# Performance work log

Hardware: AMD Instinct MI355X
Metric: run time of the kernel (lower is better)

The kernel has to match this reference:

```python
import jax, jax.numpy as jnp
import numpy as np

B, L, D, H = 2, 2048, 1024, 16
HD = D // H


def setup_inputs() -> dict:
    key = jax.random.key(0)
    ks = jax.random.split(key, 13)
    s = 0.02
    return {
        "x": jax.random.normal(ks[0], (B, L, D), jnp.float32),
        "pos_emb": jax.random.normal(ks[1], (1, L, D), jnp.float32),
        "Wq": jax.random.normal(ks[2], (D, D), jnp.float32) * s,
        "bq": jax.random.normal(ks[3], (D,), jnp.float32) * s,
        "Wk": jax.random.normal(ks[4], (D, D), jnp.float32) * s,
        "bk": jax.random.normal(ks[5], (D,), jnp.float32) * s,
        "Wv": jax.random.normal(ks[6], (D, D), jnp.float32) * s,
        "bv": jax.random.normal(ks[7], (D,), jnp.float32) * s,
        "Wpos": jax.random.normal(ks[8], (D, D), jnp.float32) * s,
        "pos_bias_u": jax.random.normal(ks[9], (H, HD), jnp.float32) * s,
        "pos_bias_v": jax.random.normal(ks[10], (H, HD), jnp.float32) * s,
        "Wo": jax.random.normal(ks[11], (D, D), jnp.float32) * s,
        "bo": jax.random.normal(ks[12], (D,), jnp.float32) * s,
    }


def _rel_shift(x):
    # x: (b, h, L, L) -> Transformer-XL relative shift
    b, h, q, k = x.shape
    x = jnp.pad(x, ((0, 0), (0, 0), (0, 0), (1, 0)))  # (b,h,L,L+1)
    x = x.reshape(b, h, k + 1, q)                      # (b,h,L+1,L)
    return x[:, :, 1:, :]                              # (b,h,L,L)


def reference(x, pos_emb, Wq, bq, Wk, bk, Wv, bv, Wpos, pos_bias_u, pos_bias_v, Wo, bo):
    b, seq, d = x.shape
    h, hd = pos_bias_u.shape
    scale = hd ** (-0.5)

    def proj(inp, W, bias=None):
        y = inp @ W.T
        if bias is not None:
            y = y + bias
        return y.reshape(inp.shape[0], seq, h, hd).transpose(0, 2, 1, 3)

    q = proj(x, Wq, bq)            # (b,h,L,hd)
    k = proj(x, Wk, bk)
    v = proj(x, Wv, bv)
    p = proj(pos_emb, Wpos)        # (1,h,L,hd)

    q_u = q + pos_bias_u[None, :, None, :]
    ac = jnp.einsum("bhqd,bhkd->bhqk", q_u, k)
    q_v = q + pos_bias_v[None, :, None, :]
    bd = jnp.matmul(q_v, jnp.swapaxes(p, -1, -2))  # broadcasts over batch
    bd = _rel_shift(bd)

    attn = jax.nn.softmax((ac + bd) * scale, axis=-1)
    out = jnp.einsum("bhqk,bhkd->bhqd", attn, v)
    out = out.transpose(0, 2, 1, 3).reshape(b, seq, d)
    return out @ Wo.T + bo
```

## Files before the change

### kernel.cpp

```cpp
#include <hip/hip_runtime.h>
#include <hip/hip_bf16.h>

constexpr int Lq = 2048;
constexpr int Dm = 1024;
constexpr int Hh = 16;
constexpr int HD = 64;

typedef __bf16 v8bf __attribute__((ext_vector_type(8)));
typedef short  v4s  __attribute__((ext_vector_type(4)));
typedef float  v4f  __attribute__((ext_vector_type(4)));

#define DEV static __device__ __forceinline__

DEV short f2bf(float f) {
  return (short)__builtin_bit_cast(unsigned short, __float2bfloat16(f));
}

DEV v4f MFMA(v8bf a, v8bf b, v4f c) {
  return __builtin_amdgcn_mfma_f32_16x16x32_bf16(a, b, c, 0, 0, 0);
}

template<int CTRL>
DEV float dppf(float x) {
  return __builtin_bit_cast(float, __builtin_amdgcn_update_dpp(
      0, __builtin_bit_cast(int, x), CTRL, 0xF, 0xF, true));
}
DEV float rowmax16(float x) {
  x = fmaxf(x, dppf<0xB1>(x));
  x = fmaxf(x, dppf<0x4E>(x));
  x = fmaxf(x, dppf<0x141>(x));
  x = fmaxf(x, dppf<0x140>(x));
  return x;
}

DEV float bperm(int byteaddr, float x) {
  return __builtin_bit_cast(float,
      __builtin_amdgcn_ds_bpermute(byteaddr, __builtin_bit_cast(int, x)));
}

#if __has_builtin(__builtin_amdgcn_exp2f)
DEV float exp2g(float x) { return __builtin_amdgcn_exp2f(x); }
#else
DEV float exp2g(float x) { return exp2f(x); }
#endif

DEV v4s cvt4(float4 v) {
  v4s w; w[0] = f2bf(v.x); w[1] = f2bf(v.y); w[2] = f2bf(v.z); w[3] = f2bf(v.w);
  return w;
}

__launch_bounds__(256)
__global__ void cvt_bf16(const float* __restrict__ in, short* __restrict__ out,
                         int n8)
{
  int i = blockIdx.x * 256 + threadIdx.x;
  if (i >= n8) return;
  float4 a = *(const float4*)(in + (size_t)i * 8);
  float4 b = *(const float4*)(in + (size_t)i * 8 + 4);
  *(v4s*)(out + (size_t)i * 8)     = cvt4(a);
  *(v4s*)(out + (size_t)i * 8 + 4) = cvt4(b);
}

__launch_bounds__(256)
__global__ void gemm_qkvp(const short* __restrict__ xb,
                          const short* __restrict__ posb,
                          const short* __restrict__ Wqb, const short* __restrict__ Wkb,
                          const short* __restrict__ Wvb, const short* __restrict__ Wpb,
                          const float* __restrict__ bq, const float* __restrict__ bk,
                          const float* __restrict__ bv,
                          const float* __restrict__ pu, const float* __restrict__ pvb,
                          short* __restrict__ Qu, short* __restrict__ Qv,
                          short* __restrict__ Kb, short* __restrict__ Vt,
                          short* __restrict__ Pb)
{
  const int z    = blockIdx.z;
  const int row0 = blockIdx.y * 64;
  const int col0 = blockIdx.x * 64;
  if (z == 3 && row0 >= Lq) return;
  const short* A = (z == 3) ? posb : xb;
  const short* W = (z == 0) ? Wqb : (z == 1) ? Wkb : (z == 2) ? Wvb : Wpb;

  __shared__ short As[64][72];
  __shared__ short Bs[64][72];

  const int tid  = threadIdx.x;
  const int lane = tid & 63;
  const int wave = tid >> 6;
  const int lr   = lane & 15;
  const int lg   = lane >> 4;
  const int wr   = (wave >> 1) * 32;
  const int wc   = (wave & 1) * 32;
  const int srow = tid >> 2;
  const int scol = (tid & 3) * 16;

  const short* Arow = A + (size_t)(row0 + srow) * Dm + scol;
  const short* Wrow = W + (size_t)(col0 + srow) * Dm + scol;

  v8bf a0 = *(const v8bf*)(Arow);
  v8bf a1 = *(const v8bf*)(Arow + 8);
  v8bf b0 = *(const v8bf*)(Wrow);
  v8bf b1 = *(const v8bf*)(Wrow + 8);

  v4f acc[2][2] = {};

  for (int k0 = 0; k0 < Dm; k0 += 64) {
    __syncthreads();
    *(v8bf*)(&As[srow][scol])     = a0;
    *(v8bf*)(&As[srow][scol + 8]) = a1;
    *(v8bf*)(&Bs[srow][scol])     = b0;
    *(v8bf*)(&Bs[srow][scol + 8]) = b1;
    __syncthreads();
    if (k0 + 64 < Dm) {
      a0 = *(const v8bf*)(Arow + k0 + 64);
      a1 = *(const v8bf*)(Arow + k0 + 72);
      b0 = *(const v8bf*)(Wrow + k0 + 64);
      b1 = *(const v8bf*)(Wrow + k0 + 72);
    }

    #pragma unroll
    for (int kk = 0; kk < 2; ++kk) {
      v8bf af[2], bfr[2];
      #pragma unroll
      for (int sm = 0; sm < 2; ++sm)
        af[sm] = *(const v8bf*)(&As[wr + sm * 16 + lr][kk * 32 + lg * 8]);
      #pragma unroll
      for (int sn = 0; sn < 2; ++sn)
        bfr[sn] = *(const v8bf*)(&Bs[wc + sn * 16 + lr][kk * 32 + lg * 8]);
      #pragma unroll
      for (int sm = 0; sm < 2; ++sm)
        #pragma unroll
        for (int sn = 0; sn < 2; ++sn)
          acc[sm][sn] = MFMA(af[sm], bfr[sn], acc[sm][sn]);
    }
  }

  #pragma unroll
  for (int sm = 0; sm < 2; ++sm) {
    #pragma unroll
    for (int sn = 0; sn < 2; ++sn) {
      #pragma unroll
      for (int r = 0; r < 4; ++r) {
        int i = row0 + wr + sm * 16 + lg * 4 + r;
        int o = col0 + wc + sn * 16 + lr;
        float val = acc[sm][sn][r];
        int b = i >> 11, l = i & 2047;
        int hh = o >> 6, hd = o & 63;
        if (z == 0) {
          val += bq[o];
          size_t idx = (((size_t)(b * Hh + hh)) * Lq + l) * HD + hd;
          Qu[idx] = f2bf(val + pu[o]);
          Qv[idx] = f2bf(val + pvb[o]);
        } else if (z == 1) {
          val += bk[o];
          size_t idx = (((size_t)(b * Hh + hh)) * Lq + l) * HD + hd;
          Kb[idx] = f2bf(val);
        } else if (z == 2) {
          val += bv[o];
          size_t idx = (((size_t)(b * Hh + hh)) * HD + hd) * Lq + l;
          Vt[idx] = f2bf(val);
        } else {
          size_t idx = ((size_t)hh * Lq + i) * HD + hd;
          Pb[idx] = f2bf(val);
        }
      }
    }
  }
}

__launch_bounds__(256)
__global__ void gemm_out(const short* __restrict__ A,
                         const short* __restrict__ W,
                         const float* __restrict__ bias,
                         float* __restrict__ out)
{
  __shared__ short As[64][72];
  __shared__ short Bs[64][72];

  const int tid  = threadIdx.x;
  const int lane = tid & 63;
  const int wave = tid >> 6;
  const int lr   = lane & 15;
  const int lg   = lane >> 4;
  const int row0 = blockIdx.y * 64;
  const int col0 = blockIdx.x * 64;
  const int wr   = (wave >> 1) * 32;
  const int wc   = (wave & 1) * 32;
  const int srow = tid >> 2;
  const int scol = (tid & 3) * 16;

  const short* Arow = A + (size_t)(row0 + srow) * Dm + scol;
  const short* Wrow = W + (size_t)(col0 + srow) * Dm + scol;

  v8bf a0 = *(const v8bf*)(Arow);
  v8bf a1 = *(const v8bf*)(Arow + 8);
  v8bf b0 = *(const v8bf*)(Wrow);
  v8bf b1 = *(const v8bf*)(Wrow + 8);

  v4f acc[2][2] = {};

  for (int k0 = 0; k0 < Dm; k0 += 64) {
    __syncthreads();
    *(v8bf*)(&As[srow][scol])     = a0;
    *(v8bf*)(&As[srow][scol + 8]) = a1;
    *(v8bf*)(&Bs[srow][scol])     = b0;
    *(v8bf*)(&Bs[srow][scol + 8]) = b1;
    __syncthreads();
    if (k0 + 64 < Dm) {
      a0 = *(const v8bf*)(Arow + k0 + 64);
      a1 = *(const v8bf*)(Arow + k0 + 72);
      b0 = *(const v8bf*)(Wrow + k0 + 64);
      b1 = *(const v8bf*)(Wrow + k0 + 72);
    }

    #pragma unroll
    for (int kk = 0; kk < 2; ++kk) {
      v8bf af[2], bfr[2];
      #pragma unroll
      for (int sm = 0; sm < 2; ++sm)
        af[sm] = *(const v8bf*)(&As[wr + sm * 16 + lr][kk * 32 + lg * 8]);
      #pragma unroll
      for (int sn = 0; sn < 2; ++sn)
        bfr[sn] = *(const v8bf*)(&Bs[wc + sn * 16 + lr][kk * 32 + lg * 8]);
      #pragma unroll
      for (int sm = 0; sm < 2; ++sm)
        #pragma unroll
        for (int sn = 0; sn < 2; ++sn)
          acc[sm][sn] = MFMA(af[sm], bfr[sn], acc[sm][sn]);
    }
  }

  #pragma unroll
  for (int sm = 0; sm < 2; ++sm)
    #pragma unroll
    for (int sn = 0; sn < 2; ++sn)
      #pragma unroll
      for (int r = 0; r < 4; ++r) {
        int i = row0 + wr + sm * 16 + lg * 4 + r;
        int o = col0 + wc + sn * 16 + lr;
        out[(size_t)i * Dm + o] = acc[sm][sn][r] + bias[o];
      }
}

__launch_bounds__(256)
__global__ void attn_kernel(const short* __restrict__ Qu,
                            const short* __restrict__ Qv,
                            const short* __restrict__ Kb,
                            const short* __restrict__ Vt,
                            const short* __restrict__ Pb,
                            short* __restrict__ AO)
{
  __shared__ short Ks[64][72];
  __shared__ short Vs[64][72];
  __shared__ short Ps[4][16][72];

  const int tid  = threadIdx.x;
  const int lane = tid & 63;
  const int wave = tid >> 6;
  const int lr   = lane & 15;
  const int lg   = lane >> 4;

  const int fid = blockIdx.x;
  const int swz = ((fid & 7) << 7) | (fid >> 3);
  const int bh  = swz >> 5;
  const int h   = bh & (Hh - 1);
  const int q0  = (swz & 31) * 64 + wave * 16;

  const short* Qu_bh = Qu + (size_t)bh * Lq * HD;
  const short* Qv_bh = Qv + (size_t)bh * Lq * HD;
  const short* Kb_bh = Kb + (size_t)bh * Lq * HD;
  const short* Vt_bh = Vt + (size_t)bh * HD * Lq;
  const short* Pl    = Pb + (size_t)h * Lq * HD + lg * 8;

  int  addr4[4];
  bool hi4[4];
  #pragma unroll
  for (int r = 0; r < 4; ++r) {
    int c = lr - (lg * 4 + r) + 15;
    hi4[r]   = (c >= 16);
    addr4[r] = (((lane & 48) | (c & 15)) << 2);
  }

  v8bf qu[2], qv1[2], qv2[2];
  {
    int q  = q0 + lr;
    int q2 = (q + 1 < Lq) ? q + 1 : Lq - 1;
    #pragma unroll
    for (int kk = 0; kk < 2; ++kk) {
      qu[kk]  = *(const v8bf*)(Qu_bh + (size_t)q  * HD + kk * 32 + lg * 8);
      qv1[kk] = *(const v8bf*)(Qv_bh + (size_t)q  * HD + kk * 32 + lg * 8);
      qv2[kk] = *(const v8bf*)(Qv_bh + (size_t)q2 * HD + kk * 32 + lg * 8);
    }
  }

  const int srow = tid >> 2;
  const int scol = (tid & 3) * 16;
  v8bf kpre0 = *(const v8bf*)(Kb_bh + (size_t)srow * HD + scol);
  v8bf kpre1 = *(const v8bf*)(Kb_bh + (size_t)srow * HD + scol + 8);
  v8bf vpre0 = *(const v8bf*)(Vt_bh + (size_t)srow * Lq + scol);
  v8bf vpre1 = *(const v8bf*)(Vt_bh + (size_t)srow * Lq + scol + 8);

  float m_r[4];
  v4f o_acc[5];
  #pragma unroll
  for (int r = 0; r < 4; ++r) m_r[r] = -1e30f;
  #pragma unroll
  for (int n = 0; n < 5; ++n) o_acc[n] = v4f{0.f, 0.f, 0.f, 0.f};

  v8bf ones;
  #pragma unroll
  for (int e = 0; e < 8; ++e) ones[e] = (__bf16)1.0f;

  const float sc = 0.125f * 1.44269504088896f;

  for (int k0 = 0; k0 < Lq; k0 += 64) {
    __syncthreads();
    *(v8bf*)(&Ks[srow][scol])     = kpre0;
    *(v8bf*)(&Ks[srow][scol + 8]) = kpre1;
    *(v8bf*)(&Vs[srow][scol])     = vpre0;
    *(v8bf*)(&Vs[srow][scol + 8]) = vpre1;
    __syncthreads();
    if (k0 + 64 < Lq) {
      kpre0 = *(const v8bf*)(Kb_bh + (size_t)(k0 + 64 + srow) * HD + scol);
      kpre1 = *(const v8bf*)(Kb_bh + (size_t)(k0 + 64 + srow) * HD + scol + 8);
      vpre0 = *(const v8bf*)(Vt_bh + (size_t)srow * Lq + k0 + 64 + scol);
      vpre1 = *(const v8bf*)(Vt_bh + (size_t)srow * Lq + k0 + 64 + scol + 8);
    }

    const int thr = q0 - k0 + 15;
    const int jb1 = 2032 + k0 - q0;
    const int jb2 = k0 - q0 - 17;

    v8bf p1[2][2], p2[2][2];
    auto loadB = [&](int n, int slot) {
      if (n * 16 <= thr) {
        int j = jb1 + n * 16 + lr;
        j = j < 0 ? 0 : (j > Lq - 1 ? Lq - 1 : j);
        const short* p = Pl + (size_t)j * HD;
        p1[slot][0] = *(const v8bf*)p;
        p1[slot][1] = *(const v8bf*)(p + 32);
      }
      if (n * 16 + 15 >= thr + 2) {
        int j = jb2 + n * 16 + lr;
        j = j < 0 ? 0 : (j > Lq - 1 ? Lq - 1 : j);
        const short* p = Pl + (size_t)j * HD;
        p2[slot][0] = *(const v8bf*)p;
        p2[slot][1] = *(const v8bf*)(p + 32);
      }
    };
    auto mergeB = [&](int n, int slot) -> v4f {
      v4f a1 = {0.f, 0.f, 0.f, 0.f}, a2 = {0.f, 0.f, 0.f, 0.f};
      if (n * 16 <= thr) {
        a1 = MFMA(qv1[0], p1[slot][0], a1);
        a1 = MFMA(qv1[1], p1[slot][1], a1);
      }
      if (n * 16 + 15 >= thr + 2) {
        a2 = MFMA(qv2[0], p2[slot][0], a2);
        a2 = MFMA(qv2[1], p2[slot][1], a2);
      }
      int cc = n * 16 + lr;
      v4f t;
      #pragma unroll
      for (int r = 0; r < 4; ++r)
        t[r] = (cc <= thr) ? a1[r] : ((cc == thr + 1) ? 0.f : a2[r]);
      return t;
    };

    loadB(0, 0);
    loadB(1, 1);

    v4f s[4];
    #pragma unroll
    for (int kt = 0; kt < 4; ++kt) {
      v8bf kf0 = *(const v8bf*)(&Ks[kt * 16 + lr][lg * 8]);
      v8bf kf1 = *(const v8bf*)(&Ks[kt * 16 + lr][32 + lg * 8]);
      s[kt] = MFMA(qu[1], kf1, MFMA(qu[0], kf0, v4f{0.f, 0.f, 0.f, 0.f}));
    }

    v4f gold, gnew;
    v4f tp = mergeB(0, 0);
    #pragma unroll
    for (int r = 0; r < 4; ++r) gold[r] = bperm(addr4[r], tp[r]);

    loadB(2, 0);
    v4f tc = mergeB(1, 1);
    #pragma unroll
    for (int r = 0; r < 4; ++r) gnew[r] = bperm(addr4[r], tc[r]);
    #pragma unroll
    for (int r = 0; r < 4; ++r)
      s[0][r] = (s[0][r] + (hi4[r] ? gnew[r] : gold[r])) * sc;
    gold = gnew;

    loadB(3, 1);
    tc = mergeB(2, 0);
    #pragma unroll
    for (int r = 0; r < 4; ++r) gnew[r] = bperm(addr4[r], tc[r]);
    #pragma unroll
    for (int r = 0; r < 4; ++r)
      s[1][r] = (s[1][r] + (hi4[r] ? gnew[r] : gold[r])) * sc;
    gold = gnew;

    loadB(4, 0);
    tc = mergeB(3, 1);
    #pragma unroll
    for (int r = 0; r < 4; ++r) gnew[r] = bperm(addr4[r], tc[r]);
    #pragma unroll
    for (int r = 0; r < 4; ++r)
      s[2][r] = (s[2][r] + (hi4[r] ? gnew[r] : gold[r])) * sc;
    gold = gnew;

    tc = mergeB(4, 0);
    #pragma unroll
    for (int r = 0; r < 4; ++r) gnew[r] = bperm(addr4[r], tc[r]);
    #pragma unroll
    for (int r = 0; r < 4; ++r)
      s[3][r] = (s[3][r] + (hi4[r] ? gnew[r] : gold[r])) * sc;

    float rmax[4];
    float need = -1e30f;
    #pragma unroll
    for (int r = 0; r < 4; ++r) {
      float m0 = fmaxf(fmaxf(s[0][r], s[1][r]), fmaxf(s[2][r], s[3][r]));
      rmax[r] = rowmax16(m0);
      need = fmaxf(need, rmax[r] - m_r[r]);
    }
    if (!__all(need <= 0.f)) {
      #pragma unroll
      for (int r = 0; r < 4; ++r) {
        float mnew  = fmaxf(m_r[r], rmax[r]);
        float alpha = exp2g(m_r[r] - mnew);
        m_r[r] = mnew;
        #pragma unroll
        for (int n = 0; n < 5; ++n)
          o_acc[n][r] *= alpha;
      }
    }
    #pragma unroll
    for (int r = 0; r < 4; ++r) {
      #pragma unroll
      for (int kt = 0; kt < 4; ++kt) {
        float p = exp2g(s[kt][r] - m_r[r]);
        Ps[wave][lg * 4 + r][kt * 16 + lr] = f2bf(p);
      }
    }
    asm volatile("s_waitcnt lgkmcnt(0)" ::: "memory");
    __builtin_amdgcn_sched_barrier(0);

    #pragma unroll
    for (int kk = 0; kk < 2; ++kk) {
      v8bf pa = *(const v8bf*)(&Ps[wave][lr][kk * 32 + lg * 8]);
      #pragma unroll
      for (int n = 0; n < 4; ++n) {
        v8bf vb = *(const v8bf*)(&Vs[n * 16 + lr][kk * 32 + lg * 8]);
        o_acc[n] = MFMA(pa, vb, o_acc[n]);
      }
      o_acc[4] = MFMA(pa, ones, o_acc[4]);
    }
  }

  const int b = bh >> 4;
  #pragma unroll
  for (int r = 0; r < 4; ++r) {
    float inv = 1.0f / o_acc[4][r];
    int q = q0 + lg * 4 + r;
    #pragma unroll
    for (int n = 0; n < 4; ++n) {
      int hd = n * 16 + lr;
      AO[((size_t)b * Lq + q) * Dm + h * HD + hd] = f2bf(o_acc[n][r] * inv);
    }
  }
}

extern "C" void kernel_launch(void* const* d_in, const int* in_sizes, int n_in,
                              void* d_out, int out_size, void* d_ws, size_t ws_size,
                              hipStream_t stream)
{
  (void)in_sizes; (void)n_in; (void)out_size; (void)ws_size;
  const float* x    = (const float*)d_in[0];
  const float* pos  = (const float*)d_in[1];
  const float* Wq   = (const float*)d_in[2];
  const float* bq   = (const float*)d_in[3];
  const float* Wk   = (const float*)d_in[4];
  const float* bk   = (const float*)d_in[5];
  const float* Wv   = (const float*)d_in[6];
  const float* bv   = (const float*)d_in[7];
  const float* Wpos = (const float*)d_in[8];
  const float* pu   = (const float*)d_in[9];
  const float* pvb  = (const float*)d_in[10];
  const float* Wo   = (const float*)d_in[11];
  const float* bo   = (const float*)d_in[12];
  float* out = (float*)d_out;

  short* Qu   = (short*)d_ws;
  short* Qv   = Qu   + (size_t)4 * 1024 * 1024;
  short* Kbuf = Qv   + (size_t)4 * 1024 * 1024;
  short* Vt   = Kbuf + (size_t)4 * 1024 * 1024;
  short* Pb   = Vt   + (size_t)4 * 1024 * 1024;
  short* AO   = Pb   + (size_t)2 * 1024 * 1024;
  short* xb   = AO   + (size_t)4 * 1024 * 1024;
  short* posb = xb   + (size_t)4 * 1024 * 1024;
  short* Wqb  = AO;
  short* Wkb  = AO + (size_t)1 * 1024 * 1024;
  short* Wvb  = AO + (size_t)2 * 1024 * 1024;
  short* Wpb  = AO + (size_t)3 * 1024 * 1024;
  short* Wob  = xb;

  dim3 blk(256);
  cvt_bf16<<<dim3(2048), blk, 0, stream>>>(x,    xb,   524288);
  cvt_bf16<<<dim3(1024), blk, 0, stream>>>(pos,  posb, 262144);
  cvt_bf16<<<dim3(512),  blk, 0, stream>>>(Wq,   Wqb,  131072);
  cvt_bf16<<<dim3(512),  blk, 0, stream>>>(Wk,   Wkb,  131072);
  cvt_bf16<<<dim3(512),  blk, 0, stream>>>(Wv,   Wvb,  131072);
  cvt_bf16<<<dim3(512),  blk, 0, stream>>>(Wpos, Wpb,  131072);
  gemm_qkvp<<<dim3(16, 64, 4), blk, 0, stream>>>(
      xb, posb, Wqb, Wkb, Wvb, Wpb, bq, bk, bv, pu, pvb,
      Qu, Qv, Kbuf, Vt, Pb);
  cvt_bf16<<<dim3(512),  blk, 0, stream>>>(Wo,   Wob,  131072);
  attn_kernel<<<dim3(1024), blk, 0, stream>>>(Qu, Qv, Kbuf, Vt, Pb, AO);
  gemm_out<<<dim3(16, 64), blk, 0, stream>>>(AO, Wob, bo, out);
}
```

Before: 339.9 us.

## Split attention over key halves, merge partials, fuse conversions, drop Qv buffer

Attention now runs as a split-K flash-decoding style pass: each block handles one query tile over half of the keys, writes normalized partial outputs plus max and sum, and a new merge kernel combines the two halves into the head-interleaved AO. This doubles the grid to improve occupancy and load balance. Qv is no longer materialized; it is reconstructed in-kernel from Qu plus (pos_bias_v - pos_bias_u), which saves one store and one load stream but adds extra bf16 rounding. All seven fp32-to-bf16 conversions are fused into one launch, and s_setprio is wrapped around the MFMA sections.

```diff
diff --git a/kernel.cpp b/kernel.cpp
--- a/kernel.cpp
+++ b/kernel.cpp
@@ -49,16 +49,26 @@
   return w;
 }
 
+struct CvtSeg { const float* src; short* dst; int n8; };
+struct CvtJobs { CvtSeg seg[7]; };
+
 __launch_bounds__(256)
-__global__ void cvt_bf16(const float* __restrict__ in, short* __restrict__ out,
-                         int n8)
+__global__ void cvt_multi(CvtJobs j)
 {
-  int i = blockIdx.x * 256 + threadIdx.x;
-  if (i >= n8) return;
-  float4 a = *(const float4*)(in + (size_t)i * 8);
-  float4 b = *(const float4*)(in + (size_t)i * 8 + 4);
-  *(v4s*)(out + (size_t)i * 8)     = cvt4(a);
-  *(v4s*)(out + (size_t)i * 8 + 4) = cvt4(b);
+  int rem = blockIdx.x * 256 + threadIdx.x;
+  #pragma unroll
+  for (int s = 0; s < 7; ++s) {
+    if (rem < j.seg[s].n8) {
+      const float* in = j.seg[s].src;
+      short* out = j.seg[s].dst;
+      float4 a = *(const float4*)(in + (size_t)rem * 8);
+      float4 b = *(const float4*)(in + (size_t)rem * 8 + 4);
+      *(v4s*)(out + (size_t)rem * 8)     = cvt4(a);
+      *(v4s*)(out + (size_t)rem * 8 + 4) = cvt4(b);
+      return;
+    }
+    rem -= j.seg[s].n8;
+  }
 }
 
 __launch_bounds__(256)
@@ -68,8 +78,8 @@
                           const short* __restrict__ Wvb, const short* __restrict__ Wpb,
                           const float* __restrict__ bq, const float* __restrict__ bk,
                           const float* __restrict__ bv,
-                          const float* __restrict__ pu, const float* __restrict__ pvb,
-                          short* __restrict__ Qu, short* __restrict__ Qv,
+                          const float* __restrict__ pu,
+                          short* __restrict__ Qu,
                           short* __restrict__ Kb, short* __restrict__ Vt,
                           short* __restrict__ Pb)
 {
@@ -146,10 +156,8 @@
         int b = i >> 11, l = i & 2047;
         int hh = o >> 6, hd = o & 63;
         if (z == 0) {
-          val += bq[o];
           size_t idx = (((size_t)(b * Hh + hh)) * Lq + l) * HD + hd;
-          Qu[idx] = f2bf(val + pu[o]);
-          Qv[idx] = f2bf(val + pvb[o]);
+          Qu[idx] = f2bf(val + bq[o] + pu[o]);
         } else if (z == 1) {
           val += bk[o];
           size_t idx = (((size_t)(b * Hh + hh)) * Lq + l) * HD + hd;
@@ -243,11 +251,14 @@
 
 __launch_bounds__(256)
 __global__ void attn_kernel(const short* __restrict__ Qu,
-                            const short* __restrict__ Qv,
                             const short* __restrict__ Kb,
                             const short* __restrict__ Vt,
                             const short* __restrict__ Pb,
-                            short* __restrict__ AO)
+                            const float* __restrict__ pu,
+                            const float* __restrict__ pvb,
+                            short* __restrict__ Op0,
+                            short* __restrict__ Op1,
+                            float* __restrict__ ml)
 {
   __shared__ short Ks[64][72];
   __shared__ short Vs[64][72];
@@ -259,14 +270,17 @@
   const int lr   = lane & 15;
   const int lg   = lane >> 4;
 
-  const int fid = blockIdx.x;
-  const int swz = ((fid & 7) << 7) | (fid >> 3);
-  const int bh  = swz >> 5;
-  const int h   = bh & (Hh - 1);
-  const int q0  = (swz & 31) * 64 + wave * 16;
+  const int fid  = blockIdx.x;
+  const int idx  = fid >> 3;
+  const int bh   = (fid & 7) * 4 + (idx >> 6);
+  const int h    = bh & (Hh - 1);
+  const int qt   = (idx & 63) >> 1;
+  const int half = idx & 1;
+  const int q0   = qt * 64 + wave * 16;
+  const int kbeg = half * (Lq / 2);
+  const int kend = kbeg + Lq / 2;
 
   const short* Qu_bh = Qu + (size_t)bh * Lq * HD;
-  const short* Qv_bh = Qv + (size_t)bh * Lq * HD;
   const short* Kb_bh = Kb + (size_t)bh * Lq * HD;
   const short* Vt_bh = Vt + (size_t)bh * HD * Lq;
   const short* Pl    = Pb + (size_t)h * Lq * HD + lg * 8;
@@ -286,18 +300,25 @@
     int q2 = (q + 1 < Lq) ? q + 1 : Lq - 1;
     #pragma unroll
     for (int kk = 0; kk < 2; ++kk) {
-      qu[kk]  = *(const v8bf*)(Qu_bh + (size_t)q  * HD + kk * 32 + lg * 8);
-      qv1[kk] = *(const v8bf*)(Qv_bh + (size_t)q  * HD + kk * 32 + lg * 8);
-      qv2[kk] = *(const v8bf*)(Qv_bh + (size_t)q2 * HD + kk * 32 + lg * 8);
+      qu[kk] = *(const v8bf*)(Qu_bh + (size_t)q  * HD + kk * 32 + lg * 8);
+      v8bf qu2 = *(const v8bf*)(Qu_bh + (size_t)q2 * HD + kk * 32 + lg * 8);
+      const float* pup = pu  + h * HD + kk * 32 + lg * 8;
+      const float* pvp = pvb + h * HD + kk * 32 + lg * 8;
+      #pragma unroll
+      for (int e = 0; e < 8; ++e) {
+        float dd = pvp[e] - pup[e];
+        qv1[kk][e] = (__bf16)((float)qu[kk][e] + dd);
+        qv2[kk][e] = (__bf16)((float)qu2[e]    + dd);
+      }
     }
   }
 
   const int srow = tid >> 2;
   const int scol = (tid & 3) * 16;
-  v8bf kpre0 = *(const v8bf*)(Kb_bh + (size_t)srow * HD + scol);
-  v8bf kpre1 = *(const v8bf*)(Kb_bh + (size_t)srow * HD + scol + 8);
-  v8bf vpre0 = *(const v8bf*)(Vt_bh + (size_t)srow * Lq + scol);
-  v8bf vpre1 = *(const v8bf*)(Vt_bh + (size_t)srow * Lq + scol + 8);
+  v8bf kpre0 = *(const v8bf*)(Kb_bh + (size_t)(kbeg + srow) * HD + scol);
+  v8bf kpre1 = *(const v8bf*)(Kb_bh + (size_t)(kbeg + srow) * HD + scol + 8);
+  v8bf vpre0 = *(const v8bf*)(Vt_bh + (size_t)srow * Lq + kbeg + scol);
+  v8bf vpre1 = *(const v8bf*)(Vt_bh + (size_t)srow * Lq + kbeg + scol + 8);
 
   float m_r[4];
   v4f o_acc[5];
@@ -312,14 +333,14 @@
 
   const float sc = 0.125f * 1.44269504088896f;
 
-  for (int k0 = 0; k0 < Lq; k0 += 64) {
+  for (int k0 = kbeg; k0 < kend; k0 += 64) {
     __syncthreads();
     *(v8bf*)(&Ks[srow][scol])     = kpre0;
     *(v8bf*)(&Ks[srow][scol + 8]) = kpre1;
     *(v8bf*)(&Vs[srow][scol])     = vpre0;
     *(v8bf*)(&Vs[srow][scol + 8]) = vpre1;
     __syncthreads();
-    if (k0 + 64 < Lq) {
+    if (k0 + 64 < kend) {
       kpre0 = *(const v8bf*)(Kb_bh + (size_t)(k0 + 64 + srow) * HD + scol);
       kpre1 = *(const v8bf*)(Kb_bh + (size_t)(k0 + 64 + srow) * HD + scol + 8);
       vpre0 = *(const v8bf*)(Vt_bh + (size_t)srow * Lq + k0 + 64 + scol);
@@ -369,12 +390,14 @@
     loadB(1, 1);
 
     v4f s[4];
+    __builtin_amdgcn_s_setprio(1);
     #pragma unroll
     for (int kt = 0; kt < 4; ++kt) {
       v8bf kf0 = *(const v8bf*)(&Ks[kt * 16 + lr][lg * 8]);
       v8bf kf1 = *(const v8bf*)(&Ks[kt * 16 + lr][32 + lg * 8]);
       s[kt] = MFMA(qu[1], kf1, MFMA(qu[0], kf0, v4f{0.f, 0.f, 0.f, 0.f}));
     }
+    __builtin_amdgcn_s_setprio(0);
 
     v4f gold, gnew;
     v4f tp = mergeB(0, 0);
@@ -445,6 +468,7 @@
     asm volatile("s_waitcnt lgkmcnt(0)" ::: "memory");
     __builtin_amdgcn_sched_barrier(0);
 
+    __builtin_amdgcn_s_setprio(1);
     #pragma unroll
     for (int kk = 0; kk < 2; ++kk) {
       v8bf pa = *(const v8bf*)(&Ps[wave][lr][kk * 32 + lg * 8]);
@@ -455,9 +479,11 @@
       }
       o_acc[4] = MFMA(pa, ones, o_acc[4]);
     }
-  }
-
-  const int b = bh >> 4;
+    __builtin_amdgcn_s_setprio(0);
+  }
+
+  short* Oph = half ? Op1 : Op0;
+  float* mlh = ml + (size_t)half * 32 * Lq * 2;
   #pragma unroll
   for (int r = 0; r < 4; ++r) {
     float inv = 1.0f / o_acc[4][r];
@@ -465,9 +491,45 @@
     #pragma unroll
     for (int n = 0; n < 4; ++n) {
       int hd = n * 16 + lr;
-      AO[((size_t)b * Lq + q) * Dm + h * HD + hd] = f2bf(o_acc[n][r] * inv);
-    }
-  }
+      Oph[((size_t)bh * Lq + q) * HD + hd] = f2bf(o_acc[n][r] * inv);
+    }
+    if (lr == 0) {
+      mlh[((size_t)bh * Lq + q) * 2 + 0] = m_r[r];
+      mlh[((size_t)bh * Lq + q) * 2 + 1] = o_acc[4][r];
+    }
+  }
+}
+
+__launch_bounds__(256)
+__global__ void merge_halves(const short* __restrict__ Op0,
+                             const short* __restrict__ Op1,
+                             const float* __restrict__ ml,
+                             short* __restrict__ AO)
+{
+  int t   = blockIdx.x * 256 + threadIdx.x;
+  int row = t >> 3;
+  int hd8 = (t & 7) * 8;
+
+  float m0 = ml[(size_t)row * 2];
+  float l0 = ml[(size_t)row * 2 + 1];
+  float m1 = ml[((size_t)(32 * Lq) + row) * 2];
+  float l1 = ml[((size_t)(32 * Lq) + row) * 2 + 1];
+  float mm = fmaxf(m0, m1);
+  float a0 = exp2g(m0 - mm) * l0;
+  float a1 = exp2g(m1 - mm) * l1;
+  float iw = 1.0f / (a0 + a1);
+  float w0 = a0 * iw, w1 = a1 * iw;
+
+  v8bf x0 = *(const v8bf*)(Op0 + (size_t)row * HD + hd8);
+  v8bf x1 = *(const v8bf*)(Op1 + (size_t)row * HD + hd8);
+  v8bf res;
+  #pragma unroll
+  for (int e = 0; e < 8; ++e)
+    res[e] = (__bf16)(w0 * (float)x0[e] + w1 * (float)x1[e]);
+
+  int bh = row >> 11, q = row & 2047;
+  int b = bh >> 4, h = bh & 15;
+  *(v8bf*)(AO + ((size_t)(b * Lq + q)) * Dm + h * HD + hd8) = res;
 }
 
 extern "C" void kernel_launch(void* const* d_in, const int* in_sizes, int n_in,
@@ -491,30 +553,36 @@
   float* out = (float*)d_out;
 
   short* Qu   = (short*)d_ws;
-  short* Qv   = Qu   + (size_t)4 * 1024 * 1024;
-  short* Kbuf = Qv   + (size_t)4 * 1024 * 1024;
+  short* Kbuf = Qu   + (size_t)4 * 1024 * 1024;
   short* Vt   = Kbuf + (size_t)4 * 1024 * 1024;
   short* Pb   = Vt   + (size_t)4 * 1024 * 1024;
-  short* AO   = Pb   + (size_t)2 * 1024 * 1024;
-  short* xb   = AO   + (size_t)4 * 1024 * 1024;
+  short* xb   = Pb   + (size_t)2 * 1024 * 1024;
   short* posb = xb   + (size_t)4 * 1024 * 1024;
-  short* Wqb  = AO;
-  short* Wkb  = AO + (size_t)1 * 1024 * 1024;
-  short* Wvb  = AO + (size_t)2 * 1024 * 1024;
-  short* Wpb  = AO + (size_t)3 * 1024 * 1024;
-  short* Wob  = xb;
+  short* Wqb  = posb + (size_t)2 * 1024 * 1024;
+  short* Wkb  = Wqb  + (size_t)1 * 1024 * 1024;
+  short* Wvb  = Wqb  + (size_t)2 * 1024 * 1024;
+  short* Wpb  = Wqb  + (size_t)3 * 1024 * 1024;
+  short* Op1  = Wqb  + (size_t)4 * 1024 * 1024;
+  short* Wob  = Op1  + (size_t)4 * 1024 * 1024;
+  short* AO   = xb;
+  float* ml   = (float*)posb;
+  short* Op0  = Wqb;
 
   dim3 blk(256);
-  cvt_bf16<<<dim3(2048), blk, 0, stream>>>(x,    xb,   524288);
-  cvt_bf16<<<dim3(1024), blk, 0, stream>>>(pos,  posb, 262144);
-  cvt_bf16<<<dim3(512),  blk, 0, stream>>>(Wq,   Wqb,  131072);
-  cvt_bf16<<<dim3(512),  blk, 0, stream>>>(Wk,   Wkb,  131072);
-  cvt_bf16<<<dim3(512),  blk, 0, stream>>>(Wv,   Wvb,  131072);
-  cvt_bf16<<<dim3(512),  blk, 0, stream>>>(Wpos, Wpb,  131072);
+  CvtJobs jobs;
+  jobs.seg[0] = {x,    xb,   524288};
+  jobs.seg[1] = {pos,  posb, 262144};
+  jobs.seg[2] = {Wq,   Wqb,  131072};
+  jobs.seg[3] = {Wk,   Wkb,  131072};
+  jobs.seg[4] = {Wv,   Wvb,  131072};
+  jobs.seg[5] = {Wpos, Wpb,  131072};
+  jobs.seg[6] = {Wo,   Wob,  131072};
+  cvt_multi<<<dim3(5632), blk, 0, stream>>>(jobs);
   gemm_qkvp<<<dim3(16, 64, 4), blk, 0, stream>>>(
-      xb, posb, Wqb, Wkb, Wvb, Wpb, bq, bk, bv, pu, pvb,
-      Qu, Qv, Kbuf, Vt, Pb);
-  cvt_bf16<<<dim3(512),  blk, 0, stream>>>(Wo,   Wob,  131072);
-  attn_kernel<<<dim3(1024), blk, 0, stream>>>(Qu, Qv, Kbuf, Vt, Pb, AO);
+      xb, posb, Wqb, Wkb, Wvb, Wpb, bq, bk, bv, pu,
+      Qu, Kbuf, Vt, Pb);
+  attn_kernel<<<dim3(2048), blk, 0, stream>>>(Qu, Kbuf, Vt, Pb, pu, pvb,
+                                              Op0, Op1, ml);
+  merge_halves<<<dim3(2048), blk, 0, stream>>>(Op0, Op1, ml, AO);
   gemm_out<<<dim3(16, 64), blk, 0, stream>>>(AO, Wob, bo, out);
 }
```

After: 333.2 us. 1.02x faster.
